# Optimization experiments

Measured on AMD Instinct MI355X. Metric: run time of the kernel, lower is better.

Reference implementation:

```python
import jax, jax.numpy as jnp
import numpy as np

B, L, D = 16384, 32, 128
DIAG_LEN, PROC_LEN, MED_LEN = 100000, 50000, 1000


def setup_inputs() -> dict:
    key = jax.random.key(0)
    ks = jax.random.split(key, 12)
    inp = {
        "diag_codes": jax.random.randint(ks[0], (B, L), 0, DIAG_LEN),
        "proc_codes": jax.random.randint(ks[1], (B, L), 0, PROC_LEN),
        "prev_diag_codes": jax.random.randint(ks[2], (B, L), 0, DIAG_LEN),
        "prev_proc_codes": jax.random.randint(ks[3], (B, L), 0, PROC_LEN),
        # learned parameters (torch Linear convention: W[out,in], y = x @ W.T + b)
        "diag_emb": jax.random.normal(ks[4], (DIAG_LEN, D), jnp.float32) * 0.02,
        "proc_emb": jax.random.normal(ks[5], (PROC_LEN, D), jnp.float32) * 0.02,
        "W1": jax.random.normal(ks[6], (D, 2 * D), jnp.float32) * 0.02,
        "b1": jnp.zeros((D,), jnp.float32),
        "W2": jax.random.normal(ks[7], (256, 2 * D), jnp.float32) * 0.02,
        "b2": jnp.zeros((256,), jnp.float32),
        "W3": jax.random.normal(ks[8], (MED_LEN, 256), jnp.float32) * 0.02,
        "b3": jnp.zeros((MED_LEN,), jnp.float32),
    }
    return inp


def _bag_sum(table, idx):
    # EmbeddingBag('sum'): gather [B,L,D] then reduce over codes -> [B,D]
    return jnp.take(table, idx, axis=0).sum(axis=1)


def reference(diag_codes, proc_codes, prev_diag_codes, prev_proc_codes,
              diag_emb, proc_emb, W1, b1, W2, b2, W3, b3):
    emb_d = _bag_sum(diag_emb, diag_codes)            # [B,128]
    emb_p = _bag_sum(proc_emb, proc_codes)            # [B,128]
    prev_d = _bag_sum(diag_emb, prev_diag_codes)      # [B,128]
    prev_p = _bag_sum(proc_emb, prev_proc_codes)      # [B,128]

    # health_net = Linear(256->128) + Dropout (identity in eval mode)
    cur = jnp.concatenate([emb_d, emb_p], axis=1) @ W1.T + b1     # [B,128]
    prev = jnp.concatenate([prev_d, prev_p], axis=1) @ W1.T + b1  # [B,128]

    rep = jnp.concatenate([cur, prev], axis=1)        # [B,256]
    h = jax.nn.relu(rep @ W2.T + b2)                  # [B,256]
    return jax.nn.sigmoid(h @ W3.T + b3)              # [B,med_len]
```

## Files before the change

kernel.cpp:

```cpp
#include <hip/hip_runtime.h>
#include <hip/hip_bf16.h>
#include <math.h>

#define NB 16384
#define MED 1000
#define MD 100000
#define MP 50000
#define TDBLK 782
#define TPBLK 391
#define NTR (TDBLK + TPBLK)
#define NCV 1280
#define FP8_SCALE 4096.0f
#define FP8_INV   (1.0f / 4096.0f)

typedef __bf16 bf16x8 __attribute__((ext_vector_type(8)));
typedef float  f32x4  __attribute__((ext_vector_type(4)));
typedef float  f32x2  __attribute__((ext_vector_type(2)));
typedef unsigned short u16;
typedef unsigned int   u32;
typedef unsigned char  u8;

__device__ __forceinline__ u16 f2bf(float f) {
    union { float f; u32 u; } v; v.f = f;
    u32 r = v.u + 0x7fffu + ((v.u >> 16) & 1u);
    return (u16)(r >> 16);
}

__global__ __launch_bounds__(256) void prep_kernel(
    const float* __restrict__ Ed, const float* __restrict__ Ep,
    const float* __restrict__ W1,
    const float* __restrict__ W2, const float* __restrict__ W3,
    u8* __restrict__ Td, u8* __restrict__ Tp,
    u16* __restrict__ W2b, u16* __restrict__ W3b)
{
    __shared__ u16 w1s[128 * 132];
    const int bid = blockIdx.x, tid = threadIdx.x;

    if (bid >= NTR) {
        int i = (bid - NTR) * 256 + tid;
        if (i < 65536) { W2b[i] = f2bf(W2[i]); return; }
        i -= 65536;
        if (i < 262144) W3b[i] = (i < MED * 256) ? f2bf(W3[i]) : (u16)0;
        return;
    }

    int blk = bid;
    const float* E; u8* T; int M, koff;
    if (blk < TDBLK) { E = Ed; T = Td; M = MD; koff = 0; }
    else             { blk -= TDBLK; E = Ep; T = Tp; M = MP; koff = 128; }

    for (int idx = tid; idx < 4096; idx += 256) {
        const int row = idx >> 5, c4 = idx & 31;
        const float4 v = *(const float4*)(W1 + row * 256 + koff + c4 * 4);
        u16* d = &w1s[row * 132 + c4 * 4];
        d[0] = f2bf(v.x); d[1] = f2bf(v.y); d[2] = f2bf(v.z); d[3] = f2bf(v.w);
    }
    __syncthreads();

    const int wave = tid >> 6, lane = tid & 63;
    const int quad = lane >> 4, l16 = lane & 15;
    const int n0 = blk * 128 + wave * 32;
    const float* bP0 = E + (size_t)min(n0 + l16,      M - 1) * 128 + quad * 8;
    const float* bP1 = E + (size_t)min(n0 + 16 + l16, M - 1) * 128 + quad * 8;

    f32x4 acc[8][2];
    #pragma unroll
    for (int mt = 0; mt < 8; ++mt) {
        acc[mt][0] = (f32x4){0.f,0.f,0.f,0.f};
        acc[mt][1] = (f32x4){0.f,0.f,0.f,0.f};
    }

    #pragma unroll
    for (int ks = 0; ks < 4; ++ks) {
        union { bf16x8 v; u16 s[8]; } b0, b1;
        const float4 f0 = *(const float4*)(bP0 + ks * 32);
        const float4 f1 = *(const float4*)(bP0 + ks * 32 + 4);
        const float4 g0 = *(const float4*)(bP1 + ks * 32);
        const float4 g1 = *(const float4*)(bP1 + ks * 32 + 4);
        b0.s[0]=f2bf(f0.x); b0.s[1]=f2bf(f0.y); b0.s[2]=f2bf(f0.z); b0.s[3]=f2bf(f0.w);
        b0.s[4]=f2bf(f1.x); b0.s[5]=f2bf(f1.y); b0.s[6]=f2bf(f1.z); b0.s[7]=f2bf(f1.w);
        b1.s[0]=f2bf(g0.x); b1.s[1]=f2bf(g0.y); b1.s[2]=f2bf(g0.z); b1.s[3]=f2bf(g0.w);
        b1.s[4]=f2bf(g1.x); b1.s[5]=f2bf(g1.y); b1.s[6]=f2bf(g1.z); b1.s[7]=f2bf(g1.w);
        #pragma unroll
        for (int mt = 0; mt < 8; ++mt) {
            const bf16x8 a = *(const bf16x8*)&w1s[(mt * 16 + l16) * 132 + ks * 32 + quad * 8];
            acc[mt][0] = __builtin_amdgcn_mfma_f32_16x16x32_bf16(a, b0.v, acc[mt][0], 0, 0, 0);
            acc[mt][1] = __builtin_amdgcn_mfma_f32_16x16x32_bf16(a, b1.v, acc[mt][1], 0, 0, 0);
        }
    }

    #pragma unroll
    for (int nt = 0; nt < 2; ++nt) {
        const int rn = n0 + nt * 16 + l16;
        if (rn < M) {
            u8* rowp = T + (size_t)rn * 128 + quad * 4;
            #pragma unroll
            for (int mt = 0; mt < 8; ++mt) {
                const f32x4 a = acc[mt][nt];
                int p = __builtin_amdgcn_cvt_pk_fp8_f32(a[0] * FP8_SCALE, a[1] * FP8_SCALE, 0, 0);
                p = __builtin_amdgcn_cvt_pk_fp8_f32(a[2] * FP8_SCALE, a[3] * FP8_SCALE, p, 1);
                *(u32*)(rowp + mt * 16) = (u32)p;
            }
        }
    }
}

__global__ __launch_bounds__(256) void gather_rep(
    const int* __restrict__ diag, const int* __restrict__ proc,
    const int* __restrict__ pdiag, const int* __restrict__ pproc,
    const u8* __restrict__ Td, const u8* __restrict__ Tp,
    const float* __restrict__ b1, u16* __restrict__ rep)
{
    __shared__ int   sidx[528];
    __shared__ float sred[128][8];
    const int t = threadIdx.x;

    for (int i = t; i < 512; i += 256) {
        const int s = i >> 7, bg = (i >> 5) & 3, l = i & 31;
        const int* cp = (bg == 0) ? diag : (bg == 1) ? proc : (bg == 2) ? pdiag : pproc;
        sidx[s * 132 + bg * 33 + l] = cp[(blockIdx.x * 4 + s) * 32 + l];
    }
    __syncthreads();

    const int sub = t >> 6, bag = (t >> 4) & 3, lc = t & 15;
    const u8* tbl = (bag & 1) ? Tp : Td;
    const int* myidx = &sidx[sub * 132 + bag * 33];

    f32x2 s0 = {0.f,0.f}, s1 = {0.f,0.f}, s2 = {0.f,0.f}, s3 = {0.f,0.f};
    uint2 va[8], vb[8];
    #pragma unroll
    for (int j = 0; j < 8; ++j)
        va[j] = *(const uint2*)(tbl + (size_t)myidx[j] * 128 + lc * 8);
    #pragma unroll
    for (int j = 0; j < 8; ++j)
        vb[j] = *(const uint2*)(tbl + (size_t)myidx[8 + j] * 128 + lc * 8);

#define CONSUME(V) do { \
    _Pragma("unroll") \
    for (int j = 0; j < 8; ++j) { \
        s0 += __builtin_amdgcn_cvt_pk_f32_fp8((int)V[j].x, 0); \
        s1 += __builtin_amdgcn_cvt_pk_f32_fp8((int)V[j].x, 1); \
        s2 += __builtin_amdgcn_cvt_pk_f32_fp8((int)V[j].y, 0); \
        s3 += __builtin_amdgcn_cvt_pk_f32_fp8((int)V[j].y, 1); \
    } } while (0)

    {
        uint2 tmp[8];
        #pragma unroll
        for (int j = 0; j < 8; ++j)
            tmp[j] = *(const uint2*)(tbl + (size_t)myidx[16 + j] * 128 + lc * 8);
        CONSUME(va);
        #pragma unroll
        for (int j = 0; j < 8; ++j) va[j] = tmp[j];
    }
    {
        uint2 tmp[8];
        #pragma unroll
        for (int j = 0; j < 8; ++j)
            tmp[j] = *(const uint2*)(tbl + (size_t)myidx[24 + j] * 128 + lc * 8);
        CONSUME(vb);
        #pragma unroll
        for (int j = 0; j < 8; ++j) vb[j] = tmp[j];
    }
    CONSUME(va);
    CONSUME(vb);
#undef CONSUME

    const int oid = sub * 32 + (bag >> 1) * 16 + lc;
    if (bag & 1) {
        *(float4*)&sred[oid][0] = make_float4(s0.x, s0.y, s1.x, s1.y);
        *(float4*)&sred[oid][4] = make_float4(s2.x, s2.y, s3.x, s3.y);
    }
    __syncthreads();
    if (!(bag & 1)) {
        const float4 p0 = *(const float4*)&sred[oid][0];
        const float4 p1 = *(const float4*)&sred[oid][4];
        const float4 c0 = *(const float4*)(b1 + lc * 8);
        const float4 c1 = *(const float4*)(b1 + lc * 8 + 4);
        const float t0 = (s0.x + p0.x) * FP8_INV + c0.x;
        const float t1 = (s0.y + p0.y) * FP8_INV + c0.y;
        const float t2 = (s1.x + p0.z) * FP8_INV + c0.z;
        const float t3 = (s1.y + p0.w) * FP8_INV + c0.w;
        const float t4 = (s2.x + p1.x) * FP8_INV + c1.x;
        const float t5 = (s2.y + p1.y) * FP8_INV + c1.y;
        const float t6 = (s3.x + p1.z) * FP8_INV + c1.z;
        const float t7 = (s3.y + p1.w) * FP8_INV + c1.w;
        uint4 o;
        o.x = (u32)f2bf(t0) | ((u32)f2bf(t1) << 16);
        o.y = (u32)f2bf(t2) | ((u32)f2bf(t3) << 16);
        o.z = (u32)f2bf(t4) | ((u32)f2bf(t5) << 16);
        o.w = (u32)f2bf(t6) | ((u32)f2bf(t7) << 16);
        const int b = blockIdx.x * 4 + sub;
        *(uint4*)(rep + (size_t)b * 256 + (bag >> 1) * 128 + lc * 8) = o;
    }
}

__global__ __launch_bounds__(256) void gemm2(
    const u16* __restrict__ rep, const u16* __restrict__ W2b,
    const float* __restrict__ b2, u16* __restrict__ h)
{
    const int wave = threadIdx.x >> 6, lane = threadIdx.x & 63;
    const int quad = lane >> 4, l16 = lane & 15;
    const int mBase = blockIdx.x * 32;
    const int nBase = wave * 64;
    const u16* aP0 = rep + (size_t)(mBase + l16) * 256 + quad * 8;
    const u16* aP1 = aP0 + 16 * 256;
    const u16* wP  = W2b + (size_t)(nBase + l16) * 256 + quad * 8;

    f32x4 acc[2][4];
    #pragma unroll
    for (int mt = 0; mt < 2; ++mt)
        #pragma unroll
        for (int nt = 0; nt < 4; ++nt) acc[mt][nt] = (f32x4){0.f,0.f,0.f,0.f};

    #pragma unroll
    for (int ks = 0; ks < 8; ++ks) {
        const bf16x8 a0 = *(const bf16x8*)(aP0 + ks * 32);
        const bf16x8 a1 = *(const bf16x8*)(aP1 + ks * 32);
        #pragma unroll
        for (int nt = 0; nt < 4; ++nt) {
            const bf16x8 b = *(const bf16x8*)(wP + nt * 16 * 256 + ks * 32);
            acc[0][nt] = __builtin_amdgcn_mfma_f32_16x16x32_bf16(a0, b, acc[0][nt], 0, 0, 0);
            acc[1][nt] = __builtin_amdgcn_mfma_f32_16x16x32_bf16(a1, b, acc[1][nt], 0, 0, 0);
        }
    }

    #pragma unroll
    for (int mt = 0; mt < 2; ++mt) {
        const int rowB = mBase + mt * 16 + quad * 4;
        #pragma unroll
        for (int nt = 0; nt < 4; ++nt) {
            const int col = nBase + nt * 16 + l16;
            const float bv = b2[col];
            #pragma unroll
            for (int r = 0; r < 4; ++r) {
                float v = acc[mt][nt][r] + bv;
                v = v > 0.f ? v : 0.f;
                h[(size_t)(rowB + r) * 256 + col] = f2bf(v);
            }
        }
    }
}

__global__ __launch_bounds__(256) void gemm3(
    const u16* __restrict__ h, const u16* __restrict__ W3b,
    const float* __restrict__ b3, float* __restrict__ out)
{
    const int wave = threadIdx.x >> 6, lane = threadIdx.x & 63;
    const int quad = lane >> 4, l16 = lane & 15;
    const int mBase = blockIdx.x * 64 + (wave & 1) * 32;
    const int nBase = blockIdx.y * 128 + (wave >> 1) * 64;
    const u16* aP0 = h + (size_t)(mBase + l16) * 256 + quad * 8;
    const u16* aP1 = aP0 + 16 * 256;
    const u16* wP  = W3b + (size_t)(nBase + l16) * 256 + quad * 8;

    f32x4 acc[2][4];
    #pragma unroll
    for (int mt = 0; mt < 2; ++mt)
        #pragma unroll
        for (int nt = 0; nt < 4; ++nt) acc[mt][nt] = (f32x4){0.f,0.f,0.f,0.f};

    #pragma unroll
    for (int ks = 0; ks < 8; ++ks) {
        const bf16x8 a0 = *(const bf16x8*)(aP0 + ks * 32);
        const bf16x8 a1 = *(const bf16x8*)(aP1 + ks * 32);
        #pragma unroll
        for (int nt = 0; nt < 4; ++nt) {
            const bf16x8 b = *(const bf16x8*)(wP + nt * 16 * 256 + ks * 32);
            acc[0][nt] = __builtin_amdgcn_mfma_f32_16x16x32_bf16(a0, b, acc[0][nt], 0, 0, 0);
            acc[1][nt] = __builtin_amdgcn_mfma_f32_16x16x32_bf16(a1, b, acc[1][nt], 0, 0, 0);
        }
    }

    #pragma unroll
    for (int nt = 0; nt < 4; ++nt) {
        const int col = nBase + nt * 16 + l16;
        if (col < MED) {
            const float bv = b3[col];
            #pragma unroll
            for (int mt = 0; mt < 2; ++mt) {
                const int rowB = mBase + mt * 16 + quad * 4;
                #pragma unroll
                for (int r = 0; r < 4; ++r) {
                    const float v = acc[mt][nt][r] + bv;
                    out[(size_t)(rowB + r) * MED + col] = 1.0f / (1.0f + __expf(-v));
                }
            }
        }
    }
}

extern "C" void kernel_launch(void* const* d_in, const int* in_sizes, int n_in,
                              void* d_out, int out_size, void* d_ws, size_t ws_size,
                              hipStream_t stream)
{
    const int*   diag  = (const int*)d_in[0];
    const int*   proc  = (const int*)d_in[1];
    const int*   pdiag = (const int*)d_in[2];
    const int*   pproc = (const int*)d_in[3];
    const float* demb  = (const float*)d_in[4];
    const float* pemb  = (const float*)d_in[5];
    const float* W1    = (const float*)d_in[6];
    const float* b1    = (const float*)d_in[7];
    const float* W2    = (const float*)d_in[8];
    const float* b2    = (const float*)d_in[9];
    const float* W3    = (const float*)d_in[10];
    const float* b3    = (const float*)d_in[11];

    char* ws = (char*)d_ws;
    u8*  Td  = (u8*)ws;
    u8*  Tp  = (u8*)(ws + 12800000);
    u16* rep = (u16*)(ws + 19200000);
    u16* W2b = (u16*)(ws + 27588608);
    u16* W3b = (u16*)(ws + 27719680);
    u16* h   = (u16*)ws;

    prep_kernel<<<NTR + NCV, 256, 0, stream>>>(demb, pemb, W1, W2, W3, Td, Tp, W2b, W3b);
    gather_rep<<<NB / 4, 256, 0, stream>>>(diag, proc, pdiag, pproc, Td, Tp, b1, rep);
    gemm2<<<512, 256, 0, stream>>>(rep, W2b, b2, h);
    gemm3<<<dim3(256, 8), 256, 0, stream>>>(h, W3b, b3, (float*)d_out);
}
```

Before: 255.3 us.

## Widen gather loads to 16 bytes, prefetch GEMM operands, use fast reciprocal

In the gather kernel each thread now loads 16-byte fp8 row chunks instead of 8, and each block covers 8 samples instead of 4. This halves the number of load instructions per gathered row and doubles per-thread register accumulators. gemm2 and gemm3 now software-prefetch the next k-step's A and B fragments before issuing the current MFMAs, to hide global load latency. The sigmoid now uses the hardware reciprocal instead of a division, which is slightly less accurate.

```diff
diff --git a/kernel.cpp b/kernel.cpp
--- a/kernel.cpp
+++ b/kernel.cpp
@@ -111,53 +111,60 @@
     const u8* __restrict__ Td, const u8* __restrict__ Tp,
     const float* __restrict__ b1, u16* __restrict__ rep)
 {
-    __shared__ int   sidx[528];
-    __shared__ float sred[128][8];
+    __shared__ int   sidx[8 * 4 * 33];
+    __shared__ float sred[8][2][8][16];
     const int t = threadIdx.x;
 
-    for (int i = t; i < 512; i += 256) {
+    for (int i = t; i < 1024; i += 256) {
         const int s = i >> 7, bg = (i >> 5) & 3, l = i & 31;
         const int* cp = (bg == 0) ? diag : (bg == 1) ? proc : (bg == 2) ? pdiag : pproc;
-        sidx[s * 132 + bg * 33 + l] = cp[(blockIdx.x * 4 + s) * 32 + l];
+        sidx[(s * 4 + bg) * 33 + l] = cp[(blockIdx.x * 8 + s) * 32 + l];
     }
     __syncthreads();
 
-    const int sub = t >> 6, bag = (t >> 4) & 3, lc = t & 15;
+    const int sub = t >> 5, bag = (t >> 3) & 3, lc = t & 7;
     const u8* tbl = (bag & 1) ? Tp : Td;
-    const int* myidx = &sidx[sub * 132 + bag * 33];
-
-    f32x2 s0 = {0.f,0.f}, s1 = {0.f,0.f}, s2 = {0.f,0.f}, s3 = {0.f,0.f};
-    uint2 va[8], vb[8];
+    const int* myidx = &sidx[(sub * 4 + bag) * 33];
+
+    f32x2 s[8];
+    #pragma unroll
+    for (int i = 0; i < 8; ++i) s[i] = (f32x2){0.f, 0.f};
+
+    uint4 va[8], vb[8];
     #pragma unroll
     for (int j = 0; j < 8; ++j)
-        va[j] = *(const uint2*)(tbl + (size_t)myidx[j] * 128 + lc * 8);
+        va[j] = *(const uint4*)(tbl + (size_t)myidx[j] * 128 + lc * 16);
     #pragma unroll
     for (int j = 0; j < 8; ++j)
-        vb[j] = *(const uint2*)(tbl + (size_t)myidx[8 + j] * 128 + lc * 8);
+        vb[j] = *(const uint4*)(tbl + (size_t)myidx[8 + j] * 128 + lc * 16);
 
 #define CONSUME(V) do { \
     _Pragma("unroll") \
     for (int j = 0; j < 8; ++j) { \
-        s0 += __builtin_amdgcn_cvt_pk_f32_fp8((int)V[j].x, 0); \
-        s1 += __builtin_amdgcn_cvt_pk_f32_fp8((int)V[j].x, 1); \
-        s2 += __builtin_amdgcn_cvt_pk_f32_fp8((int)V[j].y, 0); \
-        s3 += __builtin_amdgcn_cvt_pk_f32_fp8((int)V[j].y, 1); \
+        s[0] += __builtin_amdgcn_cvt_pk_f32_fp8((int)V[j].x, 0); \
+        s[1] += __builtin_amdgcn_cvt_pk_f32_fp8((int)V[j].x, 1); \
+        s[2] += __builtin_amdgcn_cvt_pk_f32_fp8((int)V[j].y, 0); \
+        s[3] += __builtin_amdgcn_cvt_pk_f32_fp8((int)V[j].y, 1); \
+        s[4] += __builtin_amdgcn_cvt_pk_f32_fp8((int)V[j].z, 0); \
+        s[5] += __builtin_amdgcn_cvt_pk_f32_fp8((int)V[j].z, 1); \
+        s[6] += __builtin_amdgcn_cvt_pk_f32_fp8((int)V[j].w, 0); \
+        s[7] += __builtin_amdgcn_cvt_pk_f32_fp8((int)V[j].w, 1); \
     } } while (0)
 
     {
-        uint2 tmp[8];
+        uint4 tmp[8];
         #pragma unroll
         for (int j = 0; j < 8; ++j)
-            tmp[j] = *(const uint2*)(tbl + (size_t)myidx[16 + j] * 128 + lc * 8);
+            tmp[j] = *(const uint4*)(tbl + (size_t)myidx[16 + j] * 128 + lc * 16);
         CONSUME(va);
         #pragma unroll
         for (int j = 0; j < 8; ++j) va[j] = tmp[j];
     }
     {
-        uint2 tmp[8];
+        uint4 tmp[8];
         #pragma unroll
         for (int j = 0; j < 8; ++j)
-            tmp[j] = *(const uint2*)(tbl + (size_t)myidx[24 + j] * 128 + lc * 8);
+            tmp[j] = *(const uint4*)(tbl + (size_t)myidx[24 + j] * 128 + lc * 16);
         CONSUME(vb);
         #pragma unroll
         for (int j = 0; j < 8; ++j) vb[j] = tmp[j];
@@ -166,32 +173,28 @@
     CONSUME(vb);
 #undef CONSUME
 
-    const int oid = sub * 32 + (bag >> 1) * 16 + lc;
+    const int half = bag >> 1;
     if (bag & 1) {
-        *(float4*)&sred[oid][0] = make_float4(s0.x, s0.y, s1.x, s1.y);
-        *(float4*)&sred[oid][4] = make_float4(s2.x, s2.y, s3.x, s3.y);
+        float* dst = &sred[sub][half][lc][0];
+        #pragma unroll
+        for (int i = 0; i < 4; ++i)
+            *(f32x4*)(dst + i * 4) = (f32x4){s[2*i].x, s[2*i].y, s[2*i+1].x, s[2*i+1].y};
     }
     __syncthreads();
     if (!(bag & 1)) {
-        const float4 p0 = *(const float4*)&sred[oid][0];
-        const float4 p1 = *(const float4*)&sred[oid][4];
-        const float4 c0 = *(const float4*)(b1 + lc * 8);
-        const float4 c1 = *(const float4*)(b1 + lc * 8 + 4);
-        const float t0 = (s0.x + p0.x) * FP8_INV + c0.x;
-        const float t1 = (s0.y + p0.y) * FP8_INV + c0.y;
-        const float t2 = (s1.x + p0.z) * FP8_INV + c0.z;
-        const float t3 = (s1.y + p0.w) * FP8_INV + c0.w;
-        const float t4 = (s2.x + p1.x) * FP8_INV + c1.x;
-        const float t5 = (s2.y + p1.y) * FP8_INV + c1.y;
-        const float t6 = (s3.x + p1.z) * FP8_INV + c1.z;
-        const float t7 = (s3.y + p1.w) * FP8_INV + c1.w;
-        uint4 o;
-        o.x = (u32)f2bf(t0) | ((u32)f2bf(t1) << 16);
-        o.y = (u32)f2bf(t2) | ((u32)f2bf(t3) << 16);
-        o.z = (u32)f2bf(t4) | ((u32)f2bf(t5) << 16);
-        o.w = (u32)f2bf(t6) | ((u32)f2bf(t7) << 16);
-        const int b = blockIdx.x * 4 + sub;
-        *(uint4*)(rep + (size_t)b * 256 + (bag >> 1) * 128 + lc * 8) = o;
+        const float* par = &sred[sub][half][lc][0];
+        const float* bp  = b1 + lc * 16;
+        u32 o[8];
+        #pragma unroll
+        for (int i = 0; i < 8; ++i) {
+            const float e0 = (s[i].x + par[2*i])   * FP8_INV + bp[2*i];
+            const float e1 = (s[i].y + par[2*i+1]) * FP8_INV + bp[2*i+1];
+            o[i] = (u32)f2bf(e0) | ((u32)f2bf(e1) << 16);
+        }
+        const int b = blockIdx.x * 8 + sub;
+        u16* dst = rep + (size_t)b * 256 + half * 128 + lc * 16;
+        *(uint4*)dst       = make_uint4(o[0], o[1], o[2], o[3]);
+        *(uint4*)(dst + 8) = make_uint4(o[4], o[5], o[6], o[7]);
     }
 }
 
@@ -213,16 +216,32 @@
         #pragma unroll
         for (int nt = 0; nt < 4; ++nt) acc[mt][nt] = (f32x4){0.f,0.f,0.f,0.f};
 
+    bf16x8 a0 = *(const bf16x8*)(aP0);
+    bf16x8 a1 = *(const bf16x8*)(aP1);
+    bf16x8 b[4];
+    #pragma unroll
+    for (int nt = 0; nt < 4; ++nt) b[nt] = *(const bf16x8*)(wP + nt * 4096);
+
     #pragma unroll
     for (int ks = 0; ks < 8; ++ks) {
-        const bf16x8 a0 = *(const bf16x8*)(aP0 + ks * 32);
-        const bf16x8 a1 = *(const bf16x8*)(aP1 + ks * 32);
+        bf16x8 a0n = a0, a1n = a1, bn[4];
+        #pragma unroll
+        for (int nt = 0; nt < 4; ++nt) bn[nt] = b[nt];
+        if (ks < 7) {
+            a0n = *(const bf16x8*)(aP0 + (ks + 1) * 32);
+            a1n = *(const bf16x8*)(aP1 + (ks + 1) * 32);
+            #pragma unroll
+            for (int nt = 0; nt < 4; ++nt)
+                bn[nt] = *(const bf16x8*)(wP + nt * 4096 + (ks + 1) * 32);
+        }
         #pragma unroll
         for (int nt = 0; nt < 4; ++nt) {
-            const bf16x8 b = *(const bf16x8*)(wP + nt * 16 * 256 + ks * 32);
-            acc[0][nt] = __builtin_amdgcn_mfma_f32_16x16x32_bf16(a0, b, acc[0][nt], 0, 0, 0);
-            acc[1][nt] = __builtin_amdgcn_mfma_f32_16x16x32_bf16(a1, b, acc[1][nt], 0, 0, 0);
-        }
+            acc[0][nt] = __builtin_amdgcn_mfma_f32_16x16x32_bf16(a0, b[nt], acc[0][nt], 0, 0, 0);
+            acc[1][nt] = __builtin_amdgcn_mfma_f32_16x16x32_bf16(a1, b[nt], acc[1][nt], 0, 0, 0);
+        }
+        a0 = a0n; a1 = a1n;
+        #pragma unroll
+        for (int nt = 0; nt < 4; ++nt) b[nt] = bn[nt];
     }
 
     #pragma unroll
@@ -260,16 +279,32 @@
         #pragma unroll
         for (int nt = 0; nt < 4; ++nt) acc[mt][nt] = (f32x4){0.f,0.f,0.f,0.f};
 
+    bf16x8 a0 = *(const bf16x8*)(aP0);
+    bf16x8 a1 = *(const bf16x8*)(aP1);
+    bf16x8 b[4];
+    #pragma unroll
+    for (int nt = 0; nt < 4; ++nt) b[nt] = *(const bf16x8*)(wP + nt * 4096);
+
     #pragma unroll
     for (int ks = 0; ks < 8; ++ks) {
-        const bf16x8 a0 = *(const bf16x8*)(aP0 + ks * 32);
-        const bf16x8 a1 = *(const bf16x8*)(aP1 + ks * 32);
+        bf16x8 a0n = a0, a1n = a1, bn[4];
+        #pragma unroll
+        for (int nt = 0; nt < 4; ++nt) bn[nt] = b[nt];
+        if (ks < 7) {
+            a0n = *(const bf16x8*)(aP0 + (ks + 1) * 32);
+            a1n = *(const bf16x8*)(aP1 + (ks + 1) * 32);
+            #pragma unroll
+            for (int nt = 0; nt < 4; ++nt)
+                bn[nt] = *(const bf16x8*)(wP + nt * 4096 + (ks + 1) * 32);
+        }
         #pragma unroll
         for (int nt = 0; nt < 4; ++nt) {
-            const bf16x8 b = *(const bf16x8*)(wP + nt * 16 * 256 + ks * 32);
-            acc[0][nt] = __builtin_amdgcn_mfma_f32_16x16x32_bf16(a0, b, acc[0][nt], 0, 0, 0);
-            acc[1][nt] = __builtin_amdgcn_mfma_f32_16x16x32_bf16(a1, b, acc[1][nt], 0, 0, 0);
-        }
+            acc[0][nt] = __builtin_amdgcn_mfma_f32_16x16x32_bf16(a0, b[nt], acc[0][nt], 0, 0, 0);
+            acc[1][nt] = __builtin_amdgcn_mfma_f32_16x16x32_bf16(a1, b[nt], acc[1][nt], 0, 0, 0);
+        }
+        a0 = a0n; a1 = a1n;
+        #pragma unroll
+        for (int nt = 0; nt < 4; ++nt) b[nt] = bn[nt];
     }
 
     #pragma unroll
@@ -283,7 +318,8 @@
                 #pragma unroll
                 for (int r = 0; r < 4; ++r) {
                     const float v = acc[mt][nt][r] + bv;
-                    out[(size_t)(rowB + r) * MED + col] = 1.0f / (1.0f + __expf(-v));
+                    const float e = __expf(-v);
+                    out[(size_t)(rowB + r) * MED + col] = __builtin_amdgcn_rcpf(1.0f + e);
                 }
             }
         }
@@ -316,7 +352,7 @@
     u16* h   = (u16*)ws;
 
     prep_kernel<<<NTR + NCV, 256, 0, stream>>>(demb, pemb, W1, W2, W3, Td, Tp, W2b, W3b);
-    gather_rep<<<NB / 4, 256, 0, stream>>>(diag, proc, pdiag, pproc, Td, Tp, b1, rep);
+    gather_rep<<<NB / 8, 256, 0, stream>>>(diag, proc, pdiag, pproc, Td, Tp, b1, rep);
     gemm2<<<512, 256, 0, stream>>>(rep, W2b, b2, h);
     gemm3<<<dim3(256, 8), 256, 0, stream>>>(h, W3b, b3, (float*)d_out);
 }
```

New measurement: 258.4 us. No clear change (+1.2%).
